# Kernel tuning notes

Measured on AMD Instinct MI355X. Metric: run time of the kernel, lower is better.

## Reference

```python
import jax, jax.numpy as jnp
import numpy as np

FEAT_DIM, PART_DIM, N_PARTS, N_EXPERTS, N_ALT = 384, 256, 8, 4, 4
CLUSTER_TEMP = 0.07
EXPERT_WARMUP = 8


def _ln(x, g, b, eps=1e-5):
    mu = x.mean(-1, keepdims=True)
    var = ((x - mu) ** 2).mean(-1, keepdims=True)
    return (x - mu) * jax.lax.rsqrt(var + eps) * g + b


def _l2norm(x, eps=1e-12):
    n = jnp.sqrt((x * x).sum(-1, keepdims=True))
    return x / jnp.maximum(n, eps)


def _gelu(x):
    return jax.nn.gelu(x, approximate=False)


def setup_inputs() -> dict:
    key = jax.random.key(0)
    ks = jax.random.split(key, 32)
    B, N = 256, 576
    s = lambda k, shp, sc=0.02: jax.random.normal(k, shp, jnp.float32) * sc
    inp = {
        'patch_features': jax.random.normal(ks[0], (B, N, FEAT_DIM), jnp.float32),
        'alt_idx': jax.random.randint(ks[1], (B,), 0, N_ALT, jnp.int32),
        'epoch': 0,
        # feat_proj: Linear(384,256) + LayerNorm(256) + GELU
        'w_proj': s(ks[2], (FEAT_DIM, PART_DIM)), 'b_proj': jnp.zeros((PART_DIM,)),
        'ln1_g': jnp.ones((PART_DIM,)), 'ln1_b': jnp.zeros((PART_DIM,)),
        # expert prototypes [E, K, D]
        'protos': s(ks[3], (N_EXPERTS, N_PARTS, PART_DIM)),
        # router
        'r_alt_emb': s(ks[4], (N_ALT, 64), 1.0),
        'r_wf': s(ks[5], (PART_DIM, 64)), 'r_bf': jnp.zeros((64,)),
        'r_w1': s(ks[6], (128, 64)), 'r_b1': jnp.zeros((64,)),
        'r_w2': s(ks[7], (64, N_EXPERTS)), 'r_b2': jnp.zeros((N_EXPERTS,)),
        # refine: LN + Linear(256,512) + GELU + Linear(512,256)
        'ref_ln_g': jnp.ones((PART_DIM,)), 'ref_ln_b': jnp.zeros((PART_DIM,)),
        'ref_w1': s(ks[8], (PART_DIM, 2 * PART_DIM)), 'ref_b1': jnp.zeros((2 * PART_DIM,)),
        'ref_w2': s(ks[9], (2 * PART_DIM, PART_DIM)), 'ref_b2': jnp.zeros((PART_DIM,)),
        # salience head: Linear(256,64)+GELU+Linear(64,1)+Sigmoid
        'sal_w1': s(ks[10], (PART_DIM, 64)), 'sal_b1': jnp.zeros((64,)),
        'sal_w2': s(ks[11], (64, 1)), 'sal_b2': jnp.zeros((1,)),
    }
    return inp


def reference(patch_features, alt_idx, epoch, w_proj, b_proj, ln1_g, ln1_b, protos,
              r_alt_emb, r_wf, r_bf, r_w1, r_b1, r_w2, r_b2,
              ref_ln_g, ref_ln_b, ref_w1, ref_b1, ref_w2, ref_b2,
              sal_w1, sal_b1, sal_w2, sal_b2):
    # --- feat projection ---
    feat = _gelu(_ln(patch_features @ w_proj + b_proj, ln1_g, ln1_b))  # [B,N,D]
    feat_stats = feat.mean(axis=1)  # [B,D]

    # --- router (AltitudeExpertRouter) ---
    warm = min(epoch / max(EXPERT_WARMUP, 1), 1.0)
    router_temp = 2.0 * (1.0 - warm) + 0.5 * warm
    f = jax.nn.relu(feat_stats @ r_wf + r_bf)            # [B,64]
    a = r_alt_emb[alt_idx]                               # [B,64]
    h = jax.nn.relu(jnp.concatenate([f, a], -1) @ r_w1 + r_b1)
    logits = (h @ r_w2 + r_b2) / router_temp             # [B,E]
    gate_weights = jax.nn.softmax(logits, axis=-1)

    # --- blended prototypes + soft assignment ---
    prototypes = jnp.einsum('be,ekd->bkd', gate_weights, protos)  # [B,K,D]
    sim = jnp.einsum('bnd,bkd->bnk', _l2norm(feat), _l2norm(prototypes)) / CLUSTER_TEMP
    assign = jax.nn.softmax(sim, axis=-1)                # [B,N,K]

    assign_t = jnp.swapaxes(assign, 1, 2)                # [B,K,N]
    mass = jnp.maximum(assign_t.sum(-1, keepdims=True), 1e-6)
    part_feat = jnp.einsum('bkn,bnd->bkd', assign_t, feat) / mass

    # --- refine residual ---
    r = _ln(part_feat, ref_ln_g, ref_ln_b)
    r = _gelu(r @ ref_w1 + ref_b1) @ ref_w2 + ref_b2
    part_feat = part_feat + r

    # --- salience ---
    salience = jax.nn.sigmoid(_gelu(part_feat @ sal_w1 + sal_b1) @ sal_w2 + sal_b2)[..., 0]

    return part_feat, assign, salience, feat, gate_weights


if __name__ == '__main__':
    out = reference(**setup_inputs())
    for o in out:
        print(o.shape, o.dtype)
```

## Files before the change

kernel.cpp:

```cpp
#include <hip/hip_runtime.h>
#include <hip/hip_bf16.h>
#include <math.h>

#define B_ 256
#define N_ 576
#define F_ 384
#define D_ 256
#define K_ 8

#define OFF_PART   0
#define OFF_ASSIGN 524288
#define OFF_SAL    1703936
#define OFF_FEAT   1705984
#define OFF_GATE   39454720

#define WS_STATS   0
#define WS_MACC    65536
#define WS_MASS    589824
#define WS_PROTON  591872
#define WS_BTW     1116160

using s16x8 = __attribute__((ext_vector_type(8))) short;
using f32x4 = __attribute__((ext_vector_type(4))) float;

__device__ __forceinline__ float gelu_exact(float x) {
    return 0.5f * x * (1.0f + erff(x * 0.70710678118654752f));
}

__device__ __forceinline__ unsigned short f2b(float f) {
    __hip_bfloat16 h = __float2bfloat16(f);
    unsigned short u;
    __builtin_memcpy(&u, &h, 2);
    return u;
}

__global__ void k0_zero(float* __restrict__ p, int n) {
    int i = blockIdx.x * blockDim.x + threadIdx.x;
    if (i < n) p[i] = 0.f;
}

__global__ void kB_conv(const float* __restrict__ w, unsigned short* __restrict__ bt) {
    int k = threadIdx.x;
    int n = blockIdx.x;
    bt[n * 384 + k] = f2b(w[k * 256 + n]);
}

__global__ __launch_bounds__(256, 3) void k1_rs(
    const float* __restrict__ patch, const unsigned short* __restrict__ btw,
    const float* __restrict__ bias, const float* __restrict__ g,
    const float* __restrict__ bb, float* __restrict__ feat,
    float* __restrict__ stats)
{
    __shared__ __align__(16) unsigned short As[64 * 384];
    __shared__ float rsum[4][64];
    __shared__ float rsq[4][64];
    __shared__ float muS[64], rsS[64];

    const int t = threadIdx.x;
    const int w = t >> 6;
    const int lane = t & 63;
    const int l15 = lane & 15;
    const int l4 = lane >> 4;
    const size_t rowbase = (size_t)blockIdx.x * 64;
    const int bidx = blockIdx.x / 9;

    {
        const int row = t >> 2, seg = t & 3;
        const float* src = patch + (rowbase + row) * F_ + seg * 96;
        char* As_c = (char*)As;
        const int rbase = row * 768;
        const int rs7 = (row & 7) << 4;
#pragma unroll
        for (int jj = 0; jj < 12; ++jj) {
            float4 v0 = *(const float4*)(src + jj * 8);
            float4 v1 = *(const float4*)(src + jj * 8 + 4);
            s16x8 pk;
            pk[0] = (short)f2b(v0.x); pk[1] = (short)f2b(v0.y);
            pk[2] = (short)f2b(v0.z); pk[3] = (short)f2b(v0.w);
            pk[4] = (short)f2b(v1.x); pk[5] = (short)f2b(v1.y);
            pk[6] = (short)f2b(v1.z); pk[7] = (short)f2b(v1.w);
            *(s16x8*)(As_c + rbase + ((seg * 192 + jj * 16) ^ rs7)) = pk;
        }
    }
    __syncthreads();

    f32x4 acc[4][4];
#pragma unroll
    for (int m = 0; m < 4; ++m)
#pragma unroll
        for (int n = 0; n < 4; ++n)
            acc[m][n] = (f32x4){0.f, 0.f, 0.f, 0.f};

    const char* As_r = (const char*)As;
    const int rs7v = (l15 & 7) << 4;
    const unsigned short* bcol = btw + (size_t)(w * 64 + l15) * F_ + l4 * 8;

    s16x8 pbA[4], pbB[4];
#pragma unroll
    for (int n = 0; n < 4; ++n) pbA[n] = *(const s16x8*)(bcol + n * 6144);

#pragma unroll
    for (int kk = 0; kk < 6; ++kk) {
        const int ks0 = 2 * kk, ks1 = ks0 + 1;
#pragma unroll
        for (int n = 0; n < 4; ++n)
            pbB[n] = *(const s16x8*)(bcol + n * 6144 + ks1 * 32);
        {
            s16x8 afr[4];
#pragma unroll
            for (int m = 0; m < 4; ++m)
                afr[m] = *(const s16x8*)(As_r + (m * 16 + l15) * 768 + ((ks0 * 64 + l4 * 16) ^ rs7v));
#pragma unroll
            for (int m = 0; m < 4; ++m)
#pragma unroll
                for (int n = 0; n < 4; ++n)
                    acc[m][n] = __builtin_amdgcn_mfma_f32_16x16x32_bf16(afr[m], pbA[n], acc[m][n], 0, 0, 0);
        }
        if (kk < 5) {
#pragma unroll
            for (int n = 0; n < 4; ++n)
                pbA[n] = *(const s16x8*)(bcol + n * 6144 + (ks0 + 2) * 32);
        }
        {
            s16x8 afr[4];
#pragma unroll
            for (int m = 0; m < 4; ++m)
                afr[m] = *(const s16x8*)(As_r + (m * 16 + l15) * 768 + ((ks1 * 64 + l4 * 16) ^ rs7v));
#pragma unroll
            for (int m = 0; m < 4; ++m)
#pragma unroll
                for (int n = 0; n < 4; ++n)
                    acc[m][n] = __builtin_amdgcn_mfma_f32_16x16x32_bf16(afr[m], pbB[n], acc[m][n], 0, 0, 0);
        }
    }

    float bv[4], gv[4], bbv[4];
#pragma unroll
    for (int n = 0; n < 4; ++n) {
        int col = w * 64 + n * 16 + l15;
        bv[n] = bias[col]; gv[n] = g[col]; bbv[n] = bb[col];
    }
#pragma unroll
    for (int m = 0; m < 4; ++m)
#pragma unroll
        for (int n = 0; n < 4; ++n)
#pragma unroll
            for (int r = 0; r < 4; ++r)
                acc[m][n][r] += bv[n];

    float ps[4][4], p2[4][4];
#pragma unroll
    for (int m = 0; m < 4; ++m)
#pragma unroll
        for (int r = 0; r < 4; ++r) {
            float s = 0.f, s2 = 0.f;
#pragma unroll
            for (int n = 0; n < 4; ++n) {
                float x = acc[m][n][r];
                s += x; s2 += x * x;
            }
            ps[m][r] = s; p2[m][r] = s2;
        }
#pragma unroll
    for (int m = 0; m < 4; ++m)
#pragma unroll
        for (int r = 0; r < 4; ++r) {
#pragma unroll
            for (int msk = 1; msk < 16; msk <<= 1) {
                ps[m][r] += __shfl_xor(ps[m][r], msk);
                p2[m][r] += __shfl_xor(p2[m][r], msk);
            }
        }
    if (l15 == 0) {
#pragma unroll
        for (int m = 0; m < 4; ++m)
#pragma unroll
            for (int r = 0; r < 4; ++r) {
                int row = m * 16 + l4 * 4 + r;
                rsum[w][row] = ps[m][r];
                rsq[w][row] = p2[m][r];
            }
    }
    __syncthreads();
    if (t < 64) {
        float s = rsum[0][t] + rsum[1][t] + rsum[2][t] + rsum[3][t];
        float q = rsq[0][t] + rsq[1][t] + rsq[2][t] + rsq[3][t];
        float mean = s * (1.f / 256.f);
        float var = q * (1.f / 256.f) - mean * mean;
        muS[t] = mean;
        rsS[t] = rsqrtf(var + 1e-5f);
    }
    __syncthreads();

    float cst[4] = {0.f, 0.f, 0.f, 0.f};
#pragma unroll
    for (int m = 0; m < 4; ++m)
#pragma unroll
        for (int r = 0; r < 4; ++r) {
            int row = m * 16 + l4 * 4 + r;
            float mu = muS[row], ri = rsS[row];
            float* fp = feat + (rowbase + row) * 256;
#pragma unroll
            for (int n = 0; n < 4; ++n) {
                int col = w * 64 + n * 16 + l15;
                float x = acc[m][n][r];
                float y = (x - mu) * ri * gv[n] + bbv[n];
                float z = gelu_exact(y);
                fp[col] = z;
                cst[n] += z;
            }
        }
#pragma unroll
    for (int n = 0; n < 4; ++n) {
        cst[n] += __shfl_xor(cst[n], 16);
        cst[n] += __shfl_xor(cst[n], 32);
    }
    if (l4 == 0) {
#pragma unroll
        for (int n = 0; n < 4; ++n)
            atomicAdd(&stats[bidx * 256 + w * 64 + n * 16 + l15], cst[n]);
    }
}

__global__ __launch_bounds__(256) void k3_router(
    const float* __restrict__ stats, const int* __restrict__ alt_idx,
    const int* __restrict__ epoch_p,
    const float* __restrict__ r_alt_emb, const float* __restrict__ r_wf,
    const float* __restrict__ r_bf, const float* __restrict__ r_w1,
    const float* __restrict__ r_b1, const float* __restrict__ r_w2,
    const float* __restrict__ r_b2, const float* __restrict__ protos,
    float* __restrict__ gate_out, float* __restrict__ proto_n)
{
    __shared__ float fs[256];
    __shared__ float cv[128];
    __shared__ float hb[64];
    __shared__ float lg[4];
    __shared__ float gate[4];
    __shared__ float pl[8 * 260];
    __shared__ float nrm[8];
    const int t = threadIdx.x, b = blockIdx.x;
    fs[t] = stats[b * D_ + t] * (1.f / (float)N_);
    __syncthreads();
    if (t < 64) {
        float a = 0.f;
        for (int d = 0; d < 256; ++d) a += fs[d] * r_wf[d * 64 + t];
        cv[t] = fmaxf(a + r_bf[t], 0.f);
    } else if (t < 128) {
        int alt = alt_idx[b];
        cv[t] = r_alt_emb[alt * 64 + (t - 64)];
    }
    __syncthreads();
    if (t < 64) {
        float a = 0.f;
        for (int d = 0; d < 128; ++d) a += cv[d] * r_w1[d * 64 + t];
        hb[t] = fmaxf(a + r_b1[t], 0.f);
    }
    __syncthreads();
    if (t < 4) {
        float a = 0.f;
        for (int d = 0; d < 64; ++d) a += hb[d] * r_w2[d * 4 + t];
        int ep = epoch_p[0];
        float warm = fminf((float)ep * (1.f / 8.f), 1.f);
        float temp = 2.f * (1.f - warm) + 0.5f * warm;
        lg[t] = (a + r_b2[t]) / temp;
    }
    __syncthreads();
    if (t == 0) {
        float m = fmaxf(fmaxf(lg[0], lg[1]), fmaxf(lg[2], lg[3]));
        float e0 = expf(lg[0] - m), e1 = expf(lg[1] - m);
        float e2 = expf(lg[2] - m), e3 = expf(lg[3] - m);
        float s = e0 + e1 + e2 + e3;
        gate[0] = e0 / s; gate[1] = e1 / s; gate[2] = e2 / s; gate[3] = e3 / s;
    }
    __syncthreads();
    if (t < 4) gate_out[b * 4 + t] = gate[t];
    float g0 = gate[0], g1 = gate[1], g2 = gate[2], g3 = gate[3];
#pragma unroll
    for (int k = 0; k < 8; ++k) {
        float p = g0 * protos[(0 * 8 + k) * 256 + t] + g1 * protos[(1 * 8 + k) * 256 + t]
                + g2 * protos[(2 * 8 + k) * 256 + t] + g3 * protos[(3 * 8 + k) * 256 + t];
        pl[k * 260 + t] = p;
    }
    __syncthreads();
    const int wave = t >> 6, lane = t & 63;
#pragma unroll
    for (int kk = 0; kk < 2; ++kk) {
        int k = wave * 2 + kk;
        float4 v = *(const float4*)(&pl[k * 260 + lane * 4]);
        float s2 = v.x * v.x + v.y * v.y + v.z * v.z + v.w * v.w;
#pragma unroll
        for (int m = 1; m < 64; m <<= 1) s2 += __shfl_xor(s2, m);
        if (lane == 0) nrm[k] = 1.f / fmaxf(sqrtf(s2), 1e-12f);
    }
    __syncthreads();
#pragma unroll
    for (int k = 0; k < 8; ++k)
        proto_n[((size_t)(b * 8 + k)) * 256 + t] = pl[k * 260 + t] * nrm[k];
}

__global__ __launch_bounds__(256) void k4_part(
    const float* __restrict__ feat, const float* __restrict__ proto_n,
    float* __restrict__ assign_out, float* __restrict__ macc_ws,
    float* __restrict__ mass_ws)
{
    __shared__ float pp[8 * 260];
    __shared__ float ft[16 * 260];
    __shared__ float asg[16 * 8];
    __shared__ float inrm[16];
    const int t = threadIdx.x, b = blockIdx.y;
    const int wave = t >> 6, lane = t & 63;
#pragma unroll
    for (int k = 0; k < 8; ++k) pp[k * 260 + t] = proto_n[((size_t)(b * 8 + k)) * 256 + t];
    float macc[8];
#pragma unroll
    for (int k = 0; k < 8; ++k) macc[k] = 0.f;
    float massr = 0.f;
    const int sn = t >> 4;
    const int sk = (t >> 1) & 7;
    const int hf = t & 1;
    const int lc = (t & 15) * 4;
    const int t0 = blockIdx.x * 9;
    for (int tile = t0; tile < t0 + 9; ++tile) {
        int n0 = tile * 16;
        __syncthreads();
        const float* fsrc = feat + ((size_t)(b * N_ + n0 + sn) * D_) + lc;
#pragma unroll
        for (int i = 0; i < 4; ++i) {
            float4 v = *(const float4*)(fsrc + 64 * i);
            *(float4*)(&ft[sn * 260 + lc + 64 * i]) = v;
        }
        __syncthreads();
#pragma unroll
        for (int rr = 0; rr < 4; ++rr) {
            int n = wave * 4 + rr;
            float4 v = *(const float4*)(&ft[n * 260 + lane * 4]);
            float s2 = v.x * v.x + v.y * v.y + v.z * v.z + v.w * v.w;
#pragma unroll
            for (int m = 1; m < 64; m <<= 1) s2 += __shfl_xor(s2, m);
            if (lane == 0) inrm[n] = 1.f / fmaxf(sqrtf(s2), 1e-12f);
        }
        __syncthreads();
        {
            const float4* fp = (const float4*)(&ft[sn * 260 + hf * 128]);
            const float4* qp = (const float4*)(&pp[sk * 260 + hf * 128]);
            float a = 0.f;
#pragma unroll 8
            for (int dd = 0; dd < 32; ++dd) {
                float4 fv = fp[dd], qv = qp[dd];
                a += fv.x * qv.x + fv.y * qv.y + fv.z * qv.z + fv.w * qv.w;
            }
            a += __shfl_xor(a, 1);
            float sim = a * inrm[sn] * (1.f / 0.07f);
            float m = sim;
            m = fmaxf(m, __shfl_xor(m, 2));
            m = fmaxf(m, __shfl_xor(m, 4));
            m = fmaxf(m, __shfl_xor(m, 8));
            float p = expf(sim - m);
            float s = p;
            s += __shfl_xor(s, 2);
            s += __shfl_xor(s, 4);
            s += __shfl_xor(s, 8);
            float av = p / s;
            if (hf == 0) assign_out[((size_t)(b * N_ + n0 + sn)) * 8 + sk] = av;
            asg[sn * 8 + sk] = av;
        }
        __syncthreads();
        if (t < 8) {
#pragma unroll
            for (int nn = 0; nn < 16; ++nn) massr += asg[nn * 8 + t];
        }
#pragma unroll 4
        for (int nn = 0; nn < 16; ++nn) {
            float4 a03 = *(const float4*)(&asg[nn * 8]);
            float4 a47 = *(const float4*)(&asg[nn * 8 + 4]);
            float fv = ft[nn * 260 + t];
            macc[0] += a03.x * fv; macc[1] += a03.y * fv;
            macc[2] += a03.z * fv; macc[3] += a03.w * fv;
            macc[4] += a47.x * fv; macc[5] += a47.y * fv;
            macc[6] += a47.z * fv; macc[7] += a47.w * fv;
        }
    }
#pragma unroll
    for (int k = 0; k < 8; ++k)
        atomicAdd(&macc_ws[((size_t)(b * 8 + k)) * 256 + t], macc[k]);
    if (t < 8) atomicAdd(&mass_ws[b * 8 + t], massr);
}

__global__ __launch_bounds__(256) void k5_refine(
    const float* __restrict__ macc_ws, const float* __restrict__ mass_ws,
    const float* __restrict__ ref_ln_g, const float* __restrict__ ref_ln_b,
    const float* __restrict__ ref_w1, const float* __restrict__ ref_b1,
    const float* __restrict__ ref_w2, const float* __restrict__ ref_b2,
    const float* __restrict__ sal_w1, const float* __restrict__ sal_b1,
    const float* __restrict__ sal_w2, const float* __restrict__ sal_b2,
    float* __restrict__ part_out, float* __restrict__ sal_out)
{
    __shared__ float raw[8 * 256];
    __shared__ float rn[8 * 256];
    __shared__ float h1[8 * 512];
    __shared__ float pf[8 * 256];
    __shared__ float s1[8 * 64];
    __shared__ float mu[8], rs[8];
    const int t = threadIdx.x, b = blockIdx.x;
    const int wave = t >> 6, lane = t & 63;
#pragma unroll
    for (int r = 0; r < 8; ++r) {
        float mm = fmaxf(mass_ws[b * 8 + r], 1e-6f);
        raw[r * 256 + t] = macc_ws[((size_t)(b * 8 + r)) * 256 + t] / mm;
    }
    __syncthreads();
#pragma unroll
    for (int rr = 0; rr < 2; ++rr) {
        int r = wave + rr * 4;
        float4 v = *(const float4*)(&raw[r * 256 + lane * 4]);
        float s = v.x + v.y + v.z + v.w;
        float s2 = v.x * v.x + v.y * v.y + v.z * v.z + v.w * v.w;
#pragma unroll
        for (int m = 1; m < 64; m <<= 1) { s += __shfl_xor(s, m); s2 += __shfl_xor(s2, m); }
        if (lane == 0) {
            float mean = s * (1.f / 256.f);
            float var = s2 * (1.f / 256.f) - mean * mean;
            mu[r] = mean;
            rs[r] = rsqrtf(var + 1e-5f);
        }
    }
    __syncthreads();
    {
        float gg = ref_ln_g[t], bbv = ref_ln_b[t];
#pragma unroll
        for (int r = 0; r < 8; ++r) {
            float x = raw[r * 256 + t];
            rn[r * 256 + t] = (x - mu[r]) * rs[r] * gg + bbv;
        }
    }
    __syncthreads();
    {
        float acca[8], accb[8];
#pragma unroll
        for (int r = 0; r < 8; ++r) { acca[r] = 0.f; accb[r] = 0.f; }
        for (int d = 0; d < 256; d += 4) {
            float4 rv[8];
#pragma unroll
            for (int r = 0; r < 8; ++r) rv[r] = *(const float4*)(&rn[r * 256 + d]);
            float wa0 = ref_w1[(size_t)(d + 0) * 512 + t], wb0 = ref_w1[(size_t)(d + 0) * 512 + t + 256];
            float wa1 = ref_w1[(size_t)(d + 1) * 512 + t], wb1 = ref_w1[(size_t)(d + 1) * 512 + t + 256];
            float wa2 = ref_w1[(size_t)(d + 2) * 512 + t], wb2 = ref_w1[(size_t)(d + 2) * 512 + t + 256];
            float wa3 = ref_w1[(size_t)(d + 3) * 512 + t], wb3 = ref_w1[(size_t)(d + 3) * 512 + t + 256];
#pragma unroll
            for (int r = 0; r < 8; ++r) {
                acca[r] += rv[r].x * wa0 + rv[r].y * wa1 + rv[r].z * wa2 + rv[r].w * wa3;
                accb[r] += rv[r].x * wb0 + rv[r].y * wb1 + rv[r].z * wb2 + rv[r].w * wb3;
            }
        }
        float b1a = ref_b1[t], b1b = ref_b1[t + 256];
#pragma unroll
        for (int r = 0; r < 8; ++r) {
            h1[r * 512 + t] = gelu_exact(acca[r] + b1a);
            h1[r * 512 + t + 256] = gelu_exact(accb[r] + b1b);
        }
    }
    __syncthreads();
    {
        float acc2[8];
#pragma unroll
        for (int r = 0; r < 8; ++r) acc2[r] = 0.f;
        for (int d = 0; d < 512; d += 4) {
            float4 hv[8];
#pragma unroll
            for (int r = 0; r < 8; ++r) hv[r] = *(const float4*)(&h1[r * 512 + d]);
            float w0 = ref_w2[(size_t)(d + 0) * 256 + t];
            float w1v = ref_w2[(size_t)(d + 1) * 256 + t];
            float w2v = ref_w2[(size_t)(d + 2) * 256 + t];
            float w3v = ref_w2[(size_t)(d + 3) * 256 + t];
#pragma unroll
            for (int r = 0; r < 8; ++r)
                acc2[r] += hv[r].x * w0 + hv[r].y * w1v + hv[r].z * w2v + hv[r].w * w3v;
        }
        float b2v = ref_b2[t];
#pragma unroll
        for (int r = 0; r < 8; ++r) {
            float v = raw[r * 256 + t] + acc2[r] + b2v;
            part_out[((size_t)(b * 8 + r)) * 256 + t] = v;
            pf[r * 256 + t] = v;
        }
    }
    __syncthreads();
    for (int o = t; o < 512; o += 256) {
        int r = o >> 6, j = o & 63;
        float a = 0.f;
        for (int d = 0; d < 256; d += 4) {
            float4 v = *(const float4*)(&pf[r * 256 + d]);
            a += v.x * sal_w1[(d + 0) * 64 + j] + v.y * sal_w1[(d + 1) * 64 + j]
               + v.z * sal_w1[(d + 2) * 64 + j] + v.w * sal_w1[(d + 3) * 64 + j];
        }
        s1[o] = gelu_exact(a + sal_b1[j]);
    }
    __syncthreads();
    if (t < 8) {
        float a = 0.f;
#pragma unroll 8
        for (int d = 0; d < 64; ++d) a += s1[t * 64 + d] * sal_w2[d];
        float x = a + sal_b2[0];
        sal_out[b * 8 + t] = 1.f / (1.f + expf(-x));
    }
}

extern "C" void kernel_launch(void* const* d_in, const int* in_sizes, int n_in,
                              void* d_out, int out_size, void* d_ws, size_t ws_size,
                              hipStream_t stream) {
    const float* patch    = (const float*)d_in[0];
    const int*   alt_idx  = (const int*)d_in[1];
    const int*   epoch    = (const int*)d_in[2];
    const float* w_proj   = (const float*)d_in[3];
    const float* b_proj   = (const float*)d_in[4];
    const float* ln1_g    = (const float*)d_in[5];
    const float* ln1_b    = (const float*)d_in[6];
    const float* protos   = (const float*)d_in[7];
    const float* r_alt    = (const float*)d_in[8];
    const float* r_wf     = (const float*)d_in[9];
    const float* r_bf     = (const float*)d_in[10];
    const float* r_w1     = (const float*)d_in[11];
    const float* r_b1     = (const float*)d_in[12];
    const float* r_w2     = (const float*)d_in[13];
    const float* r_b2     = (const float*)d_in[14];
    const float* ref_ln_g = (const float*)d_in[15];
    const float* ref_ln_b = (const float*)d_in[16];
    const float* ref_w1   = (const float*)d_in[17];
    const float* ref_b1   = (const float*)d_in[18];
    const float* ref_w2   = (const float*)d_in[19];
    const float* ref_b2   = (const float*)d_in[20];
    const float* sal_w1   = (const float*)d_in[21];
    const float* sal_b1   = (const float*)d_in[22];
    const float* sal_w2   = (const float*)d_in[23];
    const float* sal_b2   = (const float*)d_in[24];

    float* out = (float*)d_out;
    float* wsf = (float*)d_ws;
    float* stats   = wsf + WS_STATS;
    float* macc    = wsf + WS_MACC;
    float* mass    = wsf + WS_MASS;
    float* proto_n = wsf + WS_PROTON;
    unsigned short* btw = (unsigned short*)(wsf + WS_BTW);

    k0_zero<<<dim3((65536 + 524288 + 2048 + 255) / 256), dim3(256), 0, stream>>>(stats, 65536 + 524288 + 2048);
    kB_conv<<<dim3(256), dim3(384), 0, stream>>>(w_proj, btw);
    k1_rs<<<dim3(2304), dim3(256), 0, stream>>>(patch, btw, b_proj, ln1_g, ln1_b,
                                                out + OFF_FEAT, stats);
    k3_router<<<dim3(256), dim3(256), 0, stream>>>(stats, alt_idx, epoch, r_alt, r_wf, r_bf,
                                                   r_w1, r_b1, r_w2, r_b2, protos,
                                                   out + OFF_GATE, proto_n);
    k4_part<<<dim3(4, 256), dim3(256), 0, stream>>>(out + OFF_FEAT, proto_n,
                                                    out + OFF_ASSIGN, macc, mass);
    k5_refine<<<dim3(256), dim3(256), 0, stream>>>(macc, mass,
                                                   ref_ln_g, ref_ln_b, ref_w1, ref_b1,
                                                   ref_w2, ref_b2, sal_w1, sal_b1, sal_w2, sal_b2,
                                                   out + OFF_PART, out + OFF_SAL);
}
```

Before: 322.1 us.

## Split projection into bf16 pre-conversion plus pipelined GEMM, fuse row norms

Adds a pass that converts patch features to packed bf16 in workspace, followed by a GEMM kernel that double-buffers small 64-wide K chunks in LDS with higher occupancy instead of staging the full fp32 row tile. The projection epilogue now also computes per-row inverse L2 norms of feat, so the assignment kernel loads them rather than recomputing them with an extra sync. The converted path runs only when the workspace is large enough, falling back to the old kernel otherwise. The conversion pass adds an extra full read of the input plus a write and re-read of the bf16 copy.

Result: slower. 372.4 us (+15.6%).

```diff
diff --git a/kernel.cpp b/kernel.cpp
--- a/kernel.cpp
+++ b/kernel.cpp
@@ -18,7 +18,10 @@
 #define WS_MACC    65536
 #define WS_MASS    589824
 #define WS_PROTON  591872
-#define WS_BTW     1116160
+#define WS_INVN    1116160
+#define WS_BTW     1263616
+#define WS_APK     1312768
+#define WS_SPLIT_BYTES 134250496ull
 
 using s16x8 = __attribute__((ext_vector_type(8))) short;
 using f32x4 = __attribute__((ext_vector_type(4))) float;
@@ -45,11 +48,217 @@
     bt[n * 384 + k] = f2b(w[k * 256 + n]);
 }
 
-__global__ __launch_bounds__(256, 3) void k1_rs(
+__global__ __launch_bounds__(256) void k1a_cvt(
+    const float* __restrict__ in, unsigned short* __restrict__ apk)
+{
+    const size_t stride = (size_t)gridDim.x * 256;
+    for (size_t i = (size_t)blockIdx.x * 256 + threadIdx.x; i < 7077888; i += stride) {
+        const float* p = in + i * 8;
+        float4 v0 = *(const float4*)(p);
+        float4 v1 = *(const float4*)(p + 4);
+        s16x8 pk;
+        pk[0] = (short)f2b(v0.x); pk[1] = (short)f2b(v0.y);
+        pk[2] = (short)f2b(v0.z); pk[3] = (short)f2b(v0.w);
+        pk[4] = (short)f2b(v1.x); pk[5] = (short)f2b(v1.y);
+        pk[6] = (short)f2b(v1.z); pk[7] = (short)f2b(v1.w);
+        *(s16x8*)(apk + i * 8) = pk;
+    }
+}
+
+#define K1_EPILOGUE(FEAT, STATS, INVN, BIAS, G, BB)                                   \
+    float bv[4], gv[4], bbv[4];                                                       \
+    _Pragma("unroll")                                                                 \
+    for (int n = 0; n < 4; ++n) {                                                     \
+        int col = w * 64 + n * 16 + l15;                                              \
+        bv[n] = BIAS[col]; gv[n] = G[col]; bbv[n] = BB[col];                          \
+    }                                                                                 \
+    _Pragma("unroll")                                                                 \
+    for (int m = 0; m < 4; ++m)                                                       \
+        _Pragma("unroll")                                                             \
+        for (int n = 0; n < 4; ++n)                                                   \
+            _Pragma("unroll")                                                         \
+            for (int r = 0; r < 4; ++r)                                               \
+                acc[m][n][r] += bv[n];                                                \
+    float ps[4][4], p2[4][4];                                                         \
+    _Pragma("unroll")                                                                 \
+    for (int m = 0; m < 4; ++m)                                                       \
+        _Pragma("unroll")                                                             \
+        for (int r = 0; r < 4; ++r) {                                                 \
+            float s = 0.f, s2 = 0.f;                                                  \
+            _Pragma("unroll")                                                         \
+            for (int n = 0; n < 4; ++n) {                                             \
+                float x = acc[m][n][r];                                               \
+                s += x; s2 += x * x;                                                  \
+            }                                                                         \
+            ps[m][r] = s; p2[m][r] = s2;                                              \
+        }                                                                             \
+    _Pragma("unroll")                                                                 \
+    for (int m = 0; m < 4; ++m)                                                       \
+        _Pragma("unroll")                                                             \
+        for (int r = 0; r < 4; ++r) {                                                 \
+            _Pragma("unroll")                                                         \
+            for (int msk = 1; msk < 16; msk <<= 1) {                                  \
+                ps[m][r] += __shfl_xor(ps[m][r], msk);                                \
+                p2[m][r] += __shfl_xor(p2[m][r], msk);                                \
+            }                                                                         \
+        }                                                                             \
+    if (l15 == 0) {                                                                   \
+        _Pragma("unroll")                                                             \
+        for (int m = 0; m < 4; ++m)                                                   \
+            _Pragma("unroll")                                                         \
+            for (int r = 0; r < 4; ++r) {                                             \
+                int row = m * 16 + l4 * 4 + r;                                        \
+                rsum[w][row] = ps[m][r];                                              \
+                rsq[w][row] = p2[m][r];                                               \
+            }                                                                         \
+    }                                                                                 \
+    __syncthreads();                                                                  \
+    if (t < 64) {                                                                     \
+        float s = rsum[0][t] + rsum[1][t] + rsum[2][t] + rsum[3][t];                  \
+        float q = rsq[0][t] + rsq[1][t] + rsq[2][t] + rsq[3][t];                      \
+        float mean = s * (1.f / 256.f);                                               \
+        float var = q * (1.f / 256.f) - mean * mean;                                  \
+        muS[t] = mean;                                                                \
+        rsS[t] = rsqrtf(var + 1e-5f);                                                 \
+    }                                                                                 \
+    __syncthreads();                                                                  \
+    float cst[4] = {0.f, 0.f, 0.f, 0.f};                                              \
+    float q2[4][4];                                                                   \
+    _Pragma("unroll")                                                                 \
+    for (int m = 0; m < 4; ++m)                                                       \
+        _Pragma("unroll")                                                             \
+        for (int r = 0; r < 4; ++r) q2[m][r] = 0.f;                                   \
+    _Pragma("unroll")                                                                 \
+    for (int m = 0; m < 4; ++m)                                                       \
+        _Pragma("unroll")                                                             \
+        for (int r = 0; r < 4; ++r) {                                                 \
+            int row = m * 16 + l4 * 4 + r;                                            \
+            float mu = muS[row], ri = rsS[row];                                       \
+            float* fp = FEAT + (rowbase + row) * 256;                                 \
+            _Pragma("unroll")                                                         \
+            for (int n = 0; n < 4; ++n) {                                             \
+                int col = w * 64 + n * 16 + l15;                                      \
+                float x = acc[m][n][r];                                               \
+                float y = (x - mu) * ri * gv[n] + bbv[n];                             \
+                float z = gelu_exact(y);                                              \
+                fp[col] = z;                                                          \
+                cst[n] += z;                                                          \
+                q2[m][r] += z * z;                                                    \
+            }                                                                         \
+        }                                                                             \
+    _Pragma("unroll")                                                                 \
+    for (int n = 0; n < 4; ++n) {                                                     \
+        cst[n] += __shfl_xor(cst[n], 16);                                             \
+        cst[n] += __shfl_xor(cst[n], 32);                                             \
+    }                                                                                 \
+    if (l4 == 0) {                                                                    \
+        _Pragma("unroll")                                                             \
+        for (int n = 0; n < 4; ++n)                                                   \
+            atomicAdd(&STATS[bidx * 256 + w * 64 + n * 16 + l15], cst[n]);            \
+    }                                                                                 \
+    _Pragma("unroll")                                                                 \
+    for (int m = 0; m < 4; ++m)                                                       \
+        _Pragma("unroll")                                                             \
+        for (int r = 0; r < 4; ++r) {                                                 \
+            float q = q2[m][r];                                                       \
+            q += __shfl_xor(q, 1); q += __shfl_xor(q, 2);                             \
+            q += __shfl_xor(q, 4); q += __shfl_xor(q, 8);                             \
+            if (l15 == 0) rsum[w][m * 16 + l4 * 4 + r] = q;                           \
+        }                                                                             \
+    __syncthreads();                                                                  \
+    if (t < 64) {                                                                     \
+        float tot = rsum[0][t] + rsum[1][t] + rsum[2][t] + rsum[3][t];                \
+        INVN[rowbase + t] = 1.f / fmaxf(sqrtf(tot), 1e-12f);                          \
+    }
+
+__global__ __launch_bounds__(256, 4) void k1b_gemm(
+    const unsigned short* __restrict__ apk, const unsigned short* __restrict__ btw,
+    const float* __restrict__ bias, const float* __restrict__ g,
+    const float* __restrict__ bb, float* __restrict__ feat,
+    float* __restrict__ stats, float* __restrict__ invn)
+{
+    __shared__ __align__(16) unsigned short Ab[2][64 * 72];
+    __shared__ float rsum[4][64];
+    __shared__ float rsq[4][64];
+    __shared__ float muS[64], rsS[64];
+
+    const int t = threadIdx.x;
+    const int w = t >> 6;
+    const int lane = t & 63;
+    const int l15 = lane & 15;
+    const int l4 = lane >> 4;
+    const size_t rowbase = (size_t)blockIdx.x * 64;
+    const int bidx = blockIdx.x / 9;
+
+    f32x4 acc[4][4];
+#pragma unroll
+    for (int m = 0; m < 4; ++m)
+#pragma unroll
+        for (int n = 0; n < 4; ++n)
+            acc[m][n] = (f32x4){0.f, 0.f, 0.f, 0.f};
+
+    const int ar = t >> 2;
+    const int ak = (t & 3) * 16;
+    const unsigned short* asrc = apk + (rowbase + ar) * F_ + ak;
+    const unsigned short* bcol = btw + (size_t)(w * 64 + l15) * F_ + l4 * 8;
+
+    s16x8 pa0, pa1;
+    s16x8 pbA[4], pbB[4];
+    pa0 = *(const s16x8*)(asrc);
+    pa1 = *(const s16x8*)(asrc + 8);
+#pragma unroll
+    for (int n = 0; n < 4; ++n) pbA[n] = *(const s16x8*)(bcol + n * 6144);
+
+    for (int c = 0; c < 6; ++c) {
+        unsigned short* dst = &Ab[c & 1][ar * 72 + ak];
+        *(s16x8*)dst = pa0;
+        *(s16x8*)(dst + 8) = pa1;
+        __syncthreads();
+        if (c < 5) {
+            pa0 = *(const s16x8*)(asrc + (c + 1) * 64);
+            pa1 = *(const s16x8*)(asrc + (c + 1) * 64 + 8);
+        }
+        const unsigned short* Ar = &Ab[c & 1][0];
+#pragma unroll
+        for (int n = 0; n < 4; ++n)
+            pbB[n] = *(const s16x8*)(bcol + n * 6144 + (2 * c + 1) * 32);
+        {
+            s16x8 afr[4];
+#pragma unroll
+            for (int m = 0; m < 4; ++m)
+                afr[m] = *(const s16x8*)&Ar[(m * 16 + l15) * 72 + l4 * 8];
+#pragma unroll
+            for (int m = 0; m < 4; ++m)
+#pragma unroll
+                for (int n = 0; n < 4; ++n)
+                    acc[m][n] = __builtin_amdgcn_mfma_f32_16x16x32_bf16(afr[m], pbA[n], acc[m][n], 0, 0, 0);
+        }
+        if (c < 5) {
+#pragma unroll
+            for (int n = 0; n < 4; ++n)
+                pbA[n] = *(const s16x8*)(bcol + n * 6144 + (2 * c + 2) * 32);
+        }
+        {
+            s16x8 afr[4];
+#pragma unroll
+            for (int m = 0; m < 4; ++m)
+                afr[m] = *(const s16x8*)&Ar[(m * 16 + l15) * 72 + 32 + l4 * 8];
+#pragma unroll
+            for (int m = 0; m < 4; ++m)
+#pragma unroll
+                for (int n = 0; n < 4; ++n)
+                    acc[m][n] = __builtin_amdgcn_mfma_f32_16x16x32_bf16(afr[m], pbB[n], acc[m][n], 0, 0, 0);
+        }
+    }
+
+    K1_EPILOGUE(feat, stats, invn, bias, g, bb)
+}
+
+__global__ __launch_bounds__(256, 3) void k1_rs_f(
     const float* __restrict__ patch, const unsigned short* __restrict__ btw,
     const float* __restrict__ bias, const float* __restrict__ g,
     const float* __restrict__ bb, float* __restrict__ feat,
-    float* __restrict__ stats)
+    float* __restrict__ stats, float* __restrict__ invn)
 {
     __shared__ __align__(16) unsigned short As[64 * 384];
     __shared__ float rsum[4][64];
@@ -134,92 +343,7 @@
         }
     }
 
-    float bv[4], gv[4], bbv[4];
-#pragma unroll
-    for (int n = 0; n < 4; ++n) {
-        int col = w * 64 + n * 16 + l15;
-        bv[n] = bias[col]; gv[n] = g[col]; bbv[n] = bb[col];
-    }
-#pragma unroll
-    for (int m = 0; m < 4; ++m)
-#pragma unroll
-        for (int n = 0; n < 4; ++n)
-#pragma unroll
-            for (int r = 0; r < 4; ++r)
-                acc[m][n][r] += bv[n];
-
-    float ps[4][4], p2[4][4];
-#pragma unroll
-    for (int m = 0; m < 4; ++m)
-#pragma unroll
-        for (int r = 0; r < 4; ++r) {
-            float s = 0.f, s2 = 0.f;
-#pragma unroll
-            for (int n = 0; n < 4; ++n) {
-                float x = acc[m][n][r];
-                s += x; s2 += x * x;
-            }
-            ps[m][r] = s; p2[m][r] = s2;
-        }
-#pragma unroll
-    for (int m = 0; m < 4; ++m)
-#pragma unroll
-        for (int r = 0; r < 4; ++r) {
-#pragma unroll
-            for (int msk = 1; msk < 16; msk <<= 1) {
-                ps[m][r] += __shfl_xor(ps[m][r], msk);
-                p2[m][r] += __shfl_xor(p2[m][r], msk);
-            }
-        }
-    if (l15 == 0) {
-#pragma unroll
-        for (int m = 0; m < 4; ++m)
-#pragma unroll
-            for (int r = 0; r < 4; ++r) {
-                int row = m * 16 + l4 * 4 + r;
-                rsum[w][row] = ps[m][r];
-                rsq[w][row] = p2[m][r];
-            }
-    }
-    __syncthreads();
-    if (t < 64) {
-        float s = rsum[0][t] + rsum[1][t] + rsum[2][t] + rsum[3][t];
-        float q = rsq[0][t] + rsq[1][t] + rsq[2][t] + rsq[3][t];
-        float mean = s * (1.f / 256.f);
-        float var = q * (1.f / 256.f) - mean * mean;
-        muS[t] = mean;
-        rsS[t] = rsqrtf(var + 1e-5f);
-    }
-    __syncthreads();
-
-    float cst[4] = {0.f, 0.f, 0.f, 0.f};
-#pragma unroll
-    for (int m = 0; m < 4; ++m)
-#pragma unroll
-        for (int r = 0; r < 4; ++r) {
-            int row = m * 16 + l4 * 4 + r;
-            float mu = muS[row], ri = rsS[row];
-            float* fp = feat + (rowbase + row) * 256;
-#pragma unroll
-            for (int n = 0; n < 4; ++n) {
-                int col = w * 64 + n * 16 + l15;
-                float x = acc[m][n][r];
-                float y = (x - mu) * ri * gv[n] + bbv[n];
-                float z = gelu_exact(y);
-                fp[col] = z;
-                cst[n] += z;
-            }
-        }
-#pragma unroll
-    for (int n = 0; n < 4; ++n) {
-        cst[n] += __shfl_xor(cst[n], 16);
-        cst[n] += __shfl_xor(cst[n], 32);
-    }
-    if (l4 == 0) {
-#pragma unroll
-        for (int n = 0; n < 4; ++n)
-            atomicAdd(&stats[bidx * 256 + w * 64 + n * 16 + l15], cst[n]);
-    }
+    K1_EPILOGUE(feat, stats, invn, bias, g, bb)
 }
 
 __global__ __launch_bounds__(256) void k3_router(
@@ -300,6 +424,7 @@
 
 __global__ __launch_bounds__(256) void k4_part(
     const float* __restrict__ feat, const float* __restrict__ proto_n,
+    const float* __restrict__ invn,
     float* __restrict__ assign_out, float* __restrict__ macc_ws,
     float* __restrict__ mass_ws)
 {
@@ -308,7 +433,6 @@
     __shared__ float asg[16 * 8];
     __shared__ float inrm[16];
     const int t = threadIdx.x, b = blockIdx.y;
-    const int wave = t >> 6, lane = t & 63;
 #pragma unroll
     for (int k = 0; k < 8; ++k) pp[k * 260 + t] = proto_n[((size_t)(b * 8 + k)) * 256 + t];
     float macc[8];
@@ -329,16 +453,7 @@
             float4 v = *(const float4*)(fsrc + 64 * i);
             *(float4*)(&ft[sn * 260 + lc + 64 * i]) = v;
         }
-        __syncthreads();
-#pragma unroll
-        for (int rr = 0; rr < 4; ++rr) {
-            int n = wave * 4 + rr;
-            float4 v = *(const float4*)(&ft[n * 260 + lane * 4]);
-            float s2 = v.x * v.x + v.y * v.y + v.z * v.z + v.w * v.w;
-#pragma unroll
-            for (int m = 1; m < 64; m <<= 1) s2 += __shfl_xor(s2, m);
-            if (lane == 0) inrm[n] = 1.f / fmaxf(sqrtf(s2), 1e-12f);
-        }
+        if (t < 16) inrm[t] = invn[(size_t)b * N_ + n0 + t];
         __syncthreads();
         {
             const float4* fp = (const float4*)(&ft[sn * 260 + hf * 128]);
@@ -540,16 +655,26 @@
     float* macc    = wsf + WS_MACC;
     float* mass    = wsf + WS_MASS;
     float* proto_n = wsf + WS_PROTON;
+    float* invn    = wsf + WS_INVN;
     unsigned short* btw = (unsigned short*)(wsf + WS_BTW);
+    unsigned short* apk = (unsigned short*)(wsf + WS_APK);
 
     k0_zero<<<dim3((65536 + 524288 + 2048 + 255) / 256), dim3(256), 0, stream>>>(stats, 65536 + 524288 + 2048);
     kB_conv<<<dim3(256), dim3(384), 0, stream>>>(w_proj, btw);
-    k1_rs<<<dim3(2304), dim3(256), 0, stream>>>(patch, btw, b_proj, ln1_g, ln1_b,
-                                                out + OFF_FEAT, stats);
+
+    if (ws_size >= WS_SPLIT_BYTES) {
+        k1a_cvt<<<dim3(2048), dim3(256), 0, stream>>>(patch, apk);
+        k1b_gemm<<<dim3(2304), dim3(256), 0, stream>>>(apk, btw, b_proj, ln1_g, ln1_b,
+                                                       out + OFF_FEAT, stats, invn);
+    } else {
+        k1_rs_f<<<dim3(2304), dim3(256), 0, stream>>>(patch, btw, b_proj, ln1_g, ln1_b,
+                                                      out + OFF_FEAT, stats, invn);
+    }
+
     k3_router<<<dim3(256), dim3(256), 0, stream>>>(stats, alt_idx, epoch, r_alt, r_wf, r_bf,
                                                    r_w1, r_b1, r_w2, r_b2, protos,
                                                    out + OFF_GATE, proto_n);
-    k4_part<<<dim3(4, 256), dim3(256), 0, stream>>>(out + OFF_FEAT, proto_n,
+    k4_part<<<dim3(4, 256), dim3(256), 0, stream>>>(out + OFF_FEAT, proto_n, invn,
                                                     out + OFF_ASSIGN, macc, mass);
     k5_refine<<<dim3(256), dim3(256), 0, stream>>>(macc, mass,
                                                    ref_ln_g, ref_ln_b, ref_w1, ref_b1,
```

## Fuse feature L2 norms into projection kernel and burst patch loads

Applied to the files above, without the earlier changes.

The projection kernel now accumulates the squared norm of each GELU output row and writes the inverse L2 norm to a new workspace buffer. The assignment kernel reads those norms instead of recomputing them with a shuffle reduction and an extra barrier per tile. The patch load is also restructured into two bursts of 12 float4 loads behind a scheduling barrier, and the B-fragment double-buffer loop is flattened into a single 12-step loop. The cost is a little extra register pressure and one more block-wide sync and reduction in the projection kernel.

Result: faster. 312.8 us (-2.9%).

```diff
diff --git a/kernel.cpp b/kernel.cpp
--- a/kernel.cpp
+++ b/kernel.cpp
@@ -18,7 +18,8 @@
 #define WS_MACC    65536
 #define WS_MASS    589824
 #define WS_PROTON  591872
-#define WS_BTW     1116160
+#define WS_INVN    1116160
+#define WS_BTW     1263616
 
 using s16x8 = __attribute__((ext_vector_type(8))) short;
 using f32x4 = __attribute__((ext_vector_type(4))) float;
@@ -45,11 +46,11 @@
     bt[n * 384 + k] = f2b(w[k * 256 + n]);
 }
 
-__global__ __launch_bounds__(256, 3) void k1_rs(
+__global__ __launch_bounds__(256, 3) void k1_burst(
     const float* __restrict__ patch, const unsigned short* __restrict__ btw,
     const float* __restrict__ bias, const float* __restrict__ g,
     const float* __restrict__ bb, float* __restrict__ feat,
-    float* __restrict__ stats)
+    float* __restrict__ stats, float* __restrict__ invn)
 {
     __shared__ __align__(16) unsigned short As[64 * 384];
     __shared__ float rsum[4][64];
@@ -71,15 +72,22 @@
         const int rbase = row * 768;
         const int rs7 = (row & 7) << 4;
 #pragma unroll
-        for (int jj = 0; jj < 12; ++jj) {
-            float4 v0 = *(const float4*)(src + jj * 8);
-            float4 v1 = *(const float4*)(src + jj * 8 + 4);
-            s16x8 pk;
-            pk[0] = (short)f2b(v0.x); pk[1] = (short)f2b(v0.y);
-            pk[2] = (short)f2b(v0.z); pk[3] = (short)f2b(v0.w);
-            pk[4] = (short)f2b(v1.x); pk[5] = (short)f2b(v1.y);
-            pk[6] = (short)f2b(v1.z); pk[7] = (short)f2b(v1.w);
-            *(s16x8*)(As_c + rbase + ((seg * 192 + jj * 16) ^ rs7)) = pk;
+        for (int h = 0; h < 2; ++h) {
+            float4 pa[12];
+#pragma unroll
+            for (int j = 0; j < 12; ++j)
+                pa[j] = *(const float4*)(src + h * 48 + j * 4);
+            __builtin_amdgcn_sched_barrier(0);
+#pragma unroll
+            for (int j = 0; j < 6; ++j) {
+                float4 v0 = pa[2 * j], v1 = pa[2 * j + 1];
+                s16x8 pk;
+                pk[0] = (short)f2b(v0.x); pk[1] = (short)f2b(v0.y);
+                pk[2] = (short)f2b(v0.z); pk[3] = (short)f2b(v0.w);
+                pk[4] = (short)f2b(v1.x); pk[5] = (short)f2b(v1.y);
+                pk[6] = (short)f2b(v1.z); pk[7] = (short)f2b(v1.w);
+                *(s16x8*)(As_c + rbase + ((seg * 192 + h * 96 + j * 16) ^ rs7)) = pk;
+            }
         }
     }
     __syncthreads();
@@ -95,42 +103,40 @@
     const int rs7v = (l15 & 7) << 4;
     const unsigned short* bcol = btw + (size_t)(w * 64 + l15) * F_ + l4 * 8;
 
-    s16x8 pbA[4], pbB[4];
-#pragma unroll
-    for (int n = 0; n < 4; ++n) pbA[n] = *(const s16x8*)(bcol + n * 6144);
-
-#pragma unroll
-    for (int kk = 0; kk < 6; ++kk) {
-        const int ks0 = 2 * kk, ks1 = ks0 + 1;
-#pragma unroll
-        for (int n = 0; n < 4; ++n)
-            pbB[n] = *(const s16x8*)(bcol + n * 6144 + ks1 * 32);
-        {
-            s16x8 afr[4];
+    s16x8 pb0[4], pb1[4];
+#pragma unroll
+    for (int n = 0; n < 4; ++n) pb0[n] = *(const s16x8*)(bcol + n * 6144);
+#pragma unroll
+    for (int n = 0; n < 4; ++n) pb1[n] = *(const s16x8*)(bcol + n * 6144 + 32);
+
+#pragma unroll
+    for (int ks = 0; ks < 12; ++ks) {
+        s16x8 afr[4];
+#pragma unroll
+        for (int m = 0; m < 4; ++m)
+            afr[m] = *(const s16x8*)(As_r + (m * 16 + l15) * 768 + ((ks * 64 + l4 * 16) ^ rs7v));
+        if (ks & 1) {
 #pragma unroll
             for (int m = 0; m < 4; ++m)
-                afr[m] = *(const s16x8*)(As_r + (m * 16 + l15) * 768 + ((ks0 * 64 + l4 * 16) ^ rs7v));
+#pragma unroll
+                for (int n = 0; n < 4; ++n)
+                    acc[m][n] = __builtin_amdgcn_mfma_f32_16x16x32_bf16(afr[m], pb1[n], acc[m][n], 0, 0, 0);
+            if (ks < 10) {
+#pragma unroll
+                for (int n = 0; n < 4; ++n)
+                    pb1[n] = *(const s16x8*)(bcol + n * 6144 + (ks + 2) * 32);
+            }
+        } else {
 #pragma unroll
             for (int m = 0; m < 4; ++m)
 #pragma unroll
                 for (int n = 0; n < 4; ++n)
-                    acc[m][n] = __builtin_amdgcn_mfma_f32_16x16x32_bf16(afr[m], pbA[n], acc[m][n], 0, 0, 0);
-        }
-        if (kk < 5) {
-#pragma unroll
-            for (int n = 0; n < 4; ++n)
-                pbA[n] = *(const s16x8*)(bcol + n * 6144 + (ks0 + 2) * 32);
-        }
-        {
-            s16x8 afr[4];
-#pragma unroll
-            for (int m = 0; m < 4; ++m)
-                afr[m] = *(const s16x8*)(As_r + (m * 16 + l15) * 768 + ((ks1 * 64 + l4 * 16) ^ rs7v));
-#pragma unroll
-            for (int m = 0; m < 4; ++m)
+                    acc[m][n] = __builtin_amdgcn_mfma_f32_16x16x32_bf16(afr[m], pb0[n], acc[m][n], 0, 0, 0);
+            if (ks < 10) {
 #pragma unroll
                 for (int n = 0; n < 4; ++n)
-                    acc[m][n] = __builtin_amdgcn_mfma_f32_16x16x32_bf16(afr[m], pbB[n], acc[m][n], 0, 0, 0);
+                    pb0[n] = *(const s16x8*)(bcol + n * 6144 + (ks + 2) * 32);
+            }
         }
     }
 
@@ -193,6 +199,11 @@
     __syncthreads();
 
     float cst[4] = {0.f, 0.f, 0.f, 0.f};
+    float q2[4][4];
+#pragma unroll
+    for (int m = 0; m < 4; ++m)
+#pragma unroll
+        for (int r = 0; r < 4; ++r) q2[m][r] = 0.f;
 #pragma unroll
     for (int m = 0; m < 4; ++m)
 #pragma unroll
@@ -208,6 +219,7 @@
                 float z = gelu_exact(y);
                 fp[col] = z;
                 cst[n] += z;
+                q2[m][r] += z * z;
             }
         }
 #pragma unroll
@@ -219,6 +231,20 @@
 #pragma unroll
         for (int n = 0; n < 4; ++n)
             atomicAdd(&stats[bidx * 256 + w * 64 + n * 16 + l15], cst[n]);
+    }
+#pragma unroll
+    for (int m = 0; m < 4; ++m)
+#pragma unroll
+        for (int r = 0; r < 4; ++r) {
+            float q = q2[m][r];
+            q += __shfl_xor(q, 1); q += __shfl_xor(q, 2);
+            q += __shfl_xor(q, 4); q += __shfl_xor(q, 8);
+            if (l15 == 0) rsum[w][m * 16 + l4 * 4 + r] = q;
+        }
+    __syncthreads();
+    if (t < 64) {
+        float tot = rsum[0][t] + rsum[1][t] + rsum[2][t] + rsum[3][t];
+        invn[rowbase + t] = 1.f / fmaxf(sqrtf(tot), 1e-12f);
     }
 }
 
@@ -300,6 +326,7 @@
 
 __global__ __launch_bounds__(256) void k4_part(
     const float* __restrict__ feat, const float* __restrict__ proto_n,
+    const float* __restrict__ invn,
     float* __restrict__ assign_out, float* __restrict__ macc_ws,
     float* __restrict__ mass_ws)
 {
@@ -308,7 +335,6 @@
     __shared__ float asg[16 * 8];
     __shared__ float inrm[16];
     const int t = threadIdx.x, b = blockIdx.y;
-    const int wave = t >> 6, lane = t & 63;
 #pragma unroll
     for (int k = 0; k < 8; ++k) pp[k * 260 + t] = proto_n[((size_t)(b * 8 + k)) * 256 + t];
     float macc[8];
@@ -329,16 +355,7 @@
             float4 v = *(const float4*)(fsrc + 64 * i);
             *(float4*)(&ft[sn * 260 + lc + 64 * i]) = v;
         }
-        __syncthreads();
-#pragma unroll
-        for (int rr = 0; rr < 4; ++rr) {
-            int n = wave * 4 + rr;
-            float4 v = *(const float4*)(&ft[n * 260 + lane * 4]);
-            float s2 = v.x * v.x + v.y * v.y + v.z * v.z + v.w * v.w;
-#pragma unroll
-            for (int m = 1; m < 64; m <<= 1) s2 += __shfl_xor(s2, m);
-            if (lane == 0) inrm[n] = 1.f / fmaxf(sqrtf(s2), 1e-12f);
-        }
+        if (t < 16) inrm[t] = invn[(size_t)b * N_ + n0 + t];
         __syncthreads();
         {
             const float4* fp = (const float4*)(&ft[sn * 260 + hf * 128]);
@@ -540,16 +557,17 @@
     float* macc    = wsf + WS_MACC;
     float* mass    = wsf + WS_MASS;
     float* proto_n = wsf + WS_PROTON;
+    float* invn    = wsf + WS_INVN;
     unsigned short* btw = (unsigned short*)(wsf + WS_BTW);
 
     k0_zero<<<dim3((65536 + 524288 + 2048 + 255) / 256), dim3(256), 0, stream>>>(stats, 65536 + 524288 + 2048);
     kB_conv<<<dim3(256), dim3(384), 0, stream>>>(w_proj, btw);
-    k1_rs<<<dim3(2304), dim3(256), 0, stream>>>(patch, btw, b_proj, ln1_g, ln1_b,
-                                                out + OFF_FEAT, stats);
+    k1_burst<<<dim3(2304), dim3(256), 0, stream>>>(patch, btw, b_proj, ln1_g, ln1_b,
+                                                   out + OFF_FEAT, stats, invn);
     k3_router<<<dim3(256), dim3(256), 0, stream>>>(stats, alt_idx, epoch, r_alt, r_wf, r_bf,
                                                    r_w1, r_b1, r_w2, r_b2, protos,
                                                    out + OFF_GATE, proto_n);
-    k4_part<<<dim3(4, 256), dim3(256), 0, stream>>>(out + OFF_FEAT, proto_n,
+    k4_part<<<dim3(4, 256), dim3(256), 0, stream>>>(out + OFF_FEAT, proto_n, invn,
                                                     out + OFF_ASSIGN, macc, mass);
     k5_refine<<<dim3(256), dim3(256), 0, stream>>>(macc, mass,
                                                    ref_ln_g, ref_ln_b, ref_w1, ref_b1,
```
